# Performance work log

Hardware: AMD Instinct MI355X
Metric: run time of the kernel (lower is better)

The kernel has to match this reference:

```python
import jax, jax.numpy as jnp
import numpy as np

BATCH = 8192
N = 32
A_NUM = 5
EPS = 1e-10
ALPHA = jnp.array([0.01, 0.25, 0.5, 0.9, 0.99], dtype=jnp.float32)


def setup_inputs() -> dict:
    key = jax.random.key(0)
    ks = jax.random.split(key, 9)
    stdv = 1.0 / np.sqrt(N)
    u = lambda k, shape: jax.random.uniform(k, shape, jnp.float32, -stdv, stdv)
    L = N * (N - 1) // 2
    return {
        "inputs": jax.random.normal(ks[0], (BATCH, N, N), jnp.float32),
        "state": jax.random.normal(ks[1], (BATCH, A_NUM * N * N), jnp.float32),
        "WR_root": u(ks[2], (A_NUM,)),
        "Wt_root": u(ks[3], (1,)),
        "Wphi_root": u(ks[4], (1,)),
        "Ws_root": u(ks[5], (A_NUM,)),
        "Br": u(ks[6], (L, 1)),
        "Bt": u(ks[7], (L, 1)),
        "By": u(ks[8], (L, 1)),
    }


def _skew(Bvec, n):
    # Replicates the torch loop: row 0 is zeros; row k (k>=1) gets B[k-1 : 2k-1]
    # in its first k columns (overlapping slices of the flat parameter vector).
    b = Bvec.reshape(-1)
    r = jnp.arange(n)[:, None]
    c = jnp.arange(n)[None, :]
    idx = jnp.clip(r - 1 + c, 0, b.shape[0] - 1)  # B[k-1+j] for entry (k, j)
    L = jnp.where(c < r, b[idx], jnp.zeros((), b.dtype))
    return L - L.T


def _cayley(S, n):
    # MatrixExp in the source: (I - S)^{-1} (I + S)
    I = jnp.eye(n, dtype=S.dtype)
    return jnp.linalg.solve(I - S, I + S)


def _translate(A, Bvec, n):
    # M @ A @ M.T with M the Cayley 'exp' of the skew matrix built from Bvec.
    M = _cayley(_skew(Bvec, n), n)
    return jnp.einsum('ij,bjk,lk->bil', M, A, M)


def _nus(W_root, A, eps):
    # Weighted average over the a_num axis with weights W_root^2 / (sum + eps).
    W = W_root * W_root
    return jnp.einsum('a,banm->bnm', W / (W.sum() + eps), A)


def reference(inputs, state, WR_root, Wt_root, Wphi_root, Ws_root, Br, Bt, By):
    Mt_1 = state.reshape(-1, A_NUM, N, N)                 # [B, a, n, n]
    X = inputs.reshape(BATCH, N, N)                       # [B, n, n]

    Yt = _nus(WR_root, Mt_1, EPS)                         # [B, n, n]
    Rt = _translate(Yt, Br, N)

    at = (Wt_root[0] ** 2) / ((Wt_root ** 2 + Wphi_root ** 2).sum() + EPS)
    Tt = (1.0 - at) * X + at * Rt                         # Frechet mean FM
    Phit = _translate(Tt, Bt, N)

    # Per-j Frechet means, vectorized over the a_num axis.
    a = ALPHA[None, :, None, None]
    Mt = (1.0 - a) * Mt_1 + a * Phit[:, None, :, :]       # [B, a, n, n]

    St = _nus(Ws_root, Mt, EPS)
    Ot = _translate(St, By, N)                            # [B, n, n]

    return Ot, Mt.reshape(-1, A_NUM, N, N)
```

## Files before the change

kernel.cpp:

```cpp
#include <hip/hip_runtime.h>

#define NB 8192
#define OT_ELEMS (NB * 1024)
#define EPSF 1e-10f

typedef __attribute__((ext_vector_type(4))) float f32x4;
typedef __attribute__((ext_vector_type(8))) short s16x8;

#define WAVE_FENCE() asm volatile("s_waitcnt lgkmcnt(0)" ::: "memory")
#define MFMA_B16(A, B, C) __builtin_amdgcn_mfma_f32_16x16x32_bf16((A), (B), (C), 0, 0, 0)

__global__ void cayley_kernel(const float* __restrict__ Br,
                              const float* __restrict__ Bt,
                              const float* __restrict__ By,
                              float* __restrict__ M_out) {
  __shared__ float A[32][33];
  __shared__ float R[32][33];
  const float* B = (blockIdx.x == 0) ? Br : (blockIdx.x == 1) ? Bt : By;
  const int t = threadIdx.x;
  const int i = t >> 5, j = t & 31;
  float Lij = (j < i) ? B[i - 1 + j] : 0.0f;
  float Lji = (i < j) ? B[j - 1 + i] : 0.0f;
  float S = Lij - Lji;
  float eye = (i == j) ? 1.0f : 0.0f;
  A[i][j] = eye - S;
  R[i][j] = eye + S;
  __syncthreads();
  for (int p = 0; p < 32; ++p) {
    float f = A[i][p] / A[p][p];
    __syncthreads();
    if (i != p) {
      A[i][j] -= f * A[p][j];
      R[i][j] -= f * R[p][j];
    }
    __syncthreads();
  }
  M_out[blockIdx.x * 1024 + i * 32 + j] = R[i][j] / A[i][i];
}

__device__ __forceinline__ void cvt_hilo8(const f32x4 f0, const f32x4 f1, s16x8& hi, s16x8& lo) {
  float f[8];
#pragma unroll
  for (int e = 0; e < 4; ++e) { f[e] = f0[e]; f[4 + e] = f1[e]; }
#pragma unroll
  for (int e = 0; e < 8; ++e) {
    unsigned u = __float_as_uint(f[e]);
    hi[e] = (short)(u >> 16);
    float ah = __uint_as_float(u & 0xffff0000u);
    lo[e] = (short)(__float_as_uint(f[e] - ah) >> 16);
  }
}

__device__ __forceinline__ void read_frag_lds(const float* sb, int off, s16x8& hi, s16x8& lo) {
  f32x4 f0 = *(const f32x4*)(sb + off);
  f32x4 f1 = *(const f32x4*)(sb + off + 4);
  cvt_hilo8(f0, f1, hi, lo);
}

__device__ __forceinline__ void congruence_rt(float* sb, int lane,
                                              const s16x8 (&Mh)[2], const s16x8 (&Ml)[2],
                                              const f32x4 (&in)[4], f32x4 (&outr)[4]) {
  const int l15 = lane & 15, l4 = lane >> 4;
  const int i0 = (lane >> 3) << 2, j0 = (lane & 7) << 2;
#pragma unroll
  for (int c = 0; c < 4; ++c) {
    f32x4 colv = {in[0][c], in[1][c], in[2][c], in[3][c]};
    *(f32x4*)(sb + (j0 + c) * 36 + i0) = colv;
  }
  WAVE_FENCE();
  s16x8 Bh[2], Bl[2];
#pragma unroll
  for (int s = 0; s < 2; ++s)
    read_frag_lds(sb, (16 * s + l15) * 36 + 8 * l4, Bh[s], Bl[s]);
  WAVE_FENCE();
  f32x4 g[2][2];
#pragma unroll
  for (int ms = 0; ms < 2; ++ms)
#pragma unroll
    for (int ns = 0; ns < 2; ++ns) {
      f32x4 acc = {0.f, 0.f, 0.f, 0.f};
      acc = MFMA_B16(Ml[ms], Bh[ns], acc);
      acc = MFMA_B16(Mh[ms], Bl[ns], acc);
      acc = MFMA_B16(Mh[ms], Bh[ns], acc);
      g[ms][ns] = acc;
    }
#pragma unroll
  for (int ms = 0; ms < 2; ++ms)
#pragma unroll
    for (int ns = 0; ns < 2; ++ns)
#pragma unroll
      for (int r = 0; r < 4; ++r)
        sb[(16 * ms + 4 * l4 + r) * 36 + 16 * ns + l15] = g[ms][ns][r];
  WAVE_FENCE();
  s16x8 Ah[2], Al[2];
#pragma unroll
  for (int s = 0; s < 2; ++s)
    read_frag_lds(sb, (16 * s + l15) * 36 + 8 * l4, Ah[s], Al[s]);
  WAVE_FENCE();
  f32x4 o[2][2];
#pragma unroll
  for (int ms = 0; ms < 2; ++ms)
#pragma unroll
    for (int ns = 0; ns < 2; ++ns) {
      f32x4 acc = {0.f, 0.f, 0.f, 0.f};
      acc = MFMA_B16(Al[ms], Mh[ns], acc);
      acc = MFMA_B16(Ah[ms], Ml[ns], acc);
      acc = MFMA_B16(Ah[ms], Mh[ns], acc);
      o[ms][ns] = acc;
    }
#pragma unroll
  for (int ms = 0; ms < 2; ++ms)
#pragma unroll
    for (int ns = 0; ns < 2; ++ns)
#pragma unroll
      for (int r = 0; r < 4; ++r)
        sb[(16 * ms + 4 * l4 + r) * 36 + 16 * ns + l15] = o[ms][ns][r];
  WAVE_FENCE();
#pragma unroll
  for (int r = 0; r < 4; ++r)
    outr[r] = *(const f32x4*)(sb + (i0 + r) * 36 + j0);
  WAVE_FENCE();
}

__global__ __launch_bounds__(64) void spdsru_main(
    const float* __restrict__ X, const float* __restrict__ state,
    const float* __restrict__ WR, const float* __restrict__ Wt,
    const float* __restrict__ Wphi, const float* __restrict__ Ws,
    const float* __restrict__ Mg, float* __restrict__ out) {
  __shared__ __align__(16) float sb[1152];
  const int lane = threadIdx.x;
  const int l15 = lane & 15, l4 = lane >> 4;
  const int i0 = (lane >> 3) << 2, j0 = (lane & 7) << 2;
  const int batch = blockIdx.x;

  s16x8 Mh[3][2], Ml[3][2];
#pragma unroll
  for (int q = 0; q < 3; ++q)
#pragma unroll
    for (int s = 0; s < 2; ++s) {
      const float* p = Mg + q * 1024 + (16 * s + l15) * 32 + 8 * l4;
      cvt_hilo8(*(const f32x4*)p, *(const f32x4*)(p + 4), Mh[q][s], Ml[q][s]);
    }

  const float alpha[5] = {0.01f, 0.25f, 0.5f, 0.9f, 0.99f};
  float wr[5], va[5];
  float cP = 0.f;
  {
    float sR = 0.f, sS = 0.f, wq[5];
#pragma unroll
    for (int a = 0; a < 5; ++a) { float v = WR[a]; wr[a] = v * v; sR += v * v; }
#pragma unroll
    for (int a = 0; a < 5; ++a) { float v = Ws[a]; wq[a] = v * v; sS += v * v; }
    const float invR = 1.0f / (sR + EPSF), invS = 1.0f / (sS + EPSF);
#pragma unroll
    for (int a = 0; a < 5; ++a) {
      wr[a] *= invR;
      float w = wq[a] * invS;
      va[a] = w * (1.0f - alpha[a]);
      cP += w * alpha[a];
    }
  }
  const float wt2 = Wt[0] * Wt[0], wp2 = Wphi[0] * Wphi[0];
  const float at = wt2 / (wt2 + wp2 + EPSF);
  const float omat = 1.0f - at;

  const float* xp = X + (size_t)batch * 1024;
  f32x4 x[4];
#pragma unroll
  for (int r = 0; r < 4; ++r) x[r] = *(const f32x4*)(xp + (i0 + r) * 32 + j0);

  const float* stp = state + (size_t)batch * 5120;
  f32x4 U[4], V[4];
#pragma unroll
  for (int r = 0; r < 4; ++r) { U[r] = f32x4{0.f, 0.f, 0.f, 0.f}; V[r] = U[r]; }
#pragma unroll
  for (int a = 0; a < 5; ++a)
#pragma unroll
    for (int r = 0; r < 4; ++r) {
      const f32x4 v = *(const f32x4*)(stp + a * 1024 + (i0 + r) * 32 + j0);
      U[r] += wr[a] * v;
      V[r] += va[a] * v;
    }

  f32x4 rt[4];
  congruence_rt(sb, lane, Mh[0], Ml[0], U, rt);
  f32x4 tt[4];
#pragma unroll
  for (int r = 0; r < 4; ++r) tt[r] = omat * x[r] + at * rt[r];

  f32x4 ph[4];
  congruence_rt(sb, lane, Mh[1], Ml[1], tt, ph);

  float* outMt = out + OT_ELEMS + (size_t)batch * 5120;
#pragma unroll
  for (int a = 0; a < 5; ++a) {
    const float al = alpha[a], om = 1.0f - al;
#pragma unroll
    for (int r = 0; r < 4; ++r) {
      const f32x4 v = *(const f32x4*)(stp + a * 1024 + (i0 + r) * 32 + j0);
      f32x4 w = om * v + al * ph[r];
      *(f32x4*)(outMt + a * 1024 + (i0 + r) * 32 + j0) = w;
    }
  }

  f32x4 st[4];
#pragma unroll
  for (int r = 0; r < 4; ++r) st[r] = V[r] + cP * ph[r];
  f32x4 ot[4];
  congruence_rt(sb, lane, Mh[2], Ml[2], st, ot);

  float* outOt = out + (size_t)batch * 1024;
#pragma unroll
  for (int r = 0; r < 4; ++r)
    *(f32x4*)(outOt + (i0 + r) * 32 + j0) = ot[r];
}

extern "C" void kernel_launch(void* const* d_in, const int* in_sizes, int n_in,
                              void* d_out, int out_size, void* d_ws, size_t ws_size,
                              hipStream_t stream) {
  const float* X     = (const float*)d_in[0];
  const float* state = (const float*)d_in[1];
  const float* WR    = (const float*)d_in[2];
  const float* Wt    = (const float*)d_in[3];
  const float* Wphi  = (const float*)d_in[4];
  const float* Ws    = (const float*)d_in[5];
  const float* Br    = (const float*)d_in[6];
  const float* Bt    = (const float*)d_in[7];
  const float* By    = (const float*)d_in[8];
  float* m_ws = (float*)d_ws;
  float* outp = (float*)d_out;

  cayley_kernel<<<3, 1024, 0, stream>>>(Br, Bt, By, m_ws);
  spdsru_main<<<NB, 64, 0, stream>>>(X, state, WR, Wt, Wphi, Ws, m_ws, outp);
}
```

Baseline: 101.4 us.

## Process two batch matrices per wavefront with interleaved congruence transforms

Each 64-thread block now handles two batch entries, and the three congruence transforms run on both matrices together through two LDS buffers. This interleaves independent MFMA chains and LDS traffic, giving more instruction-level parallelism per wave and amortizing the per-block load and hi/lo split of the three M matrices. St is now accumulated from the freshly computed Mt values rather than from a precomputed V/cP decomposition. In exchange the grid is half as large, register pressure roughly doubles, and occupancy may drop.

```diff
diff --git a/kernel.cpp b/kernel.cpp
--- a/kernel.cpp
+++ b/kernel.cpp
@@ -57,68 +57,86 @@
   cvt_hilo8(f0, f1, hi, lo);
 }
 
-__device__ __forceinline__ void congruence_rt(float* sb, int lane,
-                                              const s16x8 (&Mh)[2], const s16x8 (&Ml)[2],
-                                              const f32x4 (&in)[4], f32x4 (&outr)[4]) {
+__device__ __forceinline__ void congruence2(float* __restrict__ sb0, float* __restrict__ sb1,
+                                            int lane,
+                                            const s16x8 (&Mh)[2], const s16x8 (&Ml)[2],
+                                            const f32x4 (&in0)[4], const f32x4 (&in1)[4],
+                                            f32x4 (&out0)[4], f32x4 (&out1)[4]) {
   const int l15 = lane & 15, l4 = lane >> 4;
   const int i0 = (lane >> 3) << 2, j0 = (lane & 7) << 2;
 #pragma unroll
   for (int c = 0; c < 4; ++c) {
-    f32x4 colv = {in[0][c], in[1][c], in[2][c], in[3][c]};
-    *(f32x4*)(sb + (j0 + c) * 36 + i0) = colv;
-  }
-  WAVE_FENCE();
-  s16x8 Bh[2], Bl[2];
-#pragma unroll
-  for (int s = 0; s < 2; ++s)
-    read_frag_lds(sb, (16 * s + l15) * 36 + 8 * l4, Bh[s], Bl[s]);
-  WAVE_FENCE();
-  f32x4 g[2][2];
+    f32x4 c0 = {in0[0][c], in0[1][c], in0[2][c], in0[3][c]};
+    f32x4 c1 = {in1[0][c], in1[1][c], in1[2][c], in1[3][c]};
+    *(f32x4*)(sb0 + (j0 + c) * 36 + i0) = c0;
+    *(f32x4*)(sb1 + (j0 + c) * 36 + i0) = c1;
+  }
+  WAVE_FENCE();
+  s16x8 Bh[2][2], Bl[2][2];
+#pragma unroll
+  for (int s = 0; s < 2; ++s) {
+    read_frag_lds(sb0, (16 * s + l15) * 36 + 8 * l4, Bh[0][s], Bl[0][s]);
+    read_frag_lds(sb1, (16 * s + l15) * 36 + 8 * l4, Bh[1][s], Bl[1][s]);
+  }
+  WAVE_FENCE();
+  f32x4 g[2][2][2];
+#pragma unroll
+  for (int b = 0; b < 2; ++b)
+#pragma unroll
+    for (int ms = 0; ms < 2; ++ms)
+#pragma unroll
+      for (int ns = 0; ns < 2; ++ns) {
+        f32x4 acc = {0.f, 0.f, 0.f, 0.f};
+        acc = MFMA_B16(Ml[ms], Bh[b][ns], acc);
+        acc = MFMA_B16(Mh[ms], Bl[b][ns], acc);
+        acc = MFMA_B16(Mh[ms], Bh[b][ns], acc);
+        g[b][ms][ns] = acc;
+      }
 #pragma unroll
   for (int ms = 0; ms < 2; ++ms)
 #pragma unroll
-    for (int ns = 0; ns < 2; ++ns) {
-      f32x4 acc = {0.f, 0.f, 0.f, 0.f};
-      acc = MFMA_B16(Ml[ms], Bh[ns], acc);
-      acc = MFMA_B16(Mh[ms], Bl[ns], acc);
-      acc = MFMA_B16(Mh[ms], Bh[ns], acc);
-      g[ms][ns] = acc;
-    }
+    for (int ns = 0; ns < 2; ++ns)
+#pragma unroll
+      for (int r = 0; r < 4; ++r) {
+        sb0[(16 * ms + 4 * l4 + r) * 36 + 16 * ns + l15] = g[0][ms][ns][r];
+        sb1[(16 * ms + 4 * l4 + r) * 36 + 16 * ns + l15] = g[1][ms][ns][r];
+      }
+  WAVE_FENCE();
+  s16x8 Ah[2][2], Al[2][2];
+#pragma unroll
+  for (int s = 0; s < 2; ++s) {
+    read_frag_lds(sb0, (16 * s + l15) * 36 + 8 * l4, Ah[0][s], Al[0][s]);
+    read_frag_lds(sb1, (16 * s + l15) * 36 + 8 * l4, Ah[1][s], Al[1][s]);
+  }
+  WAVE_FENCE();
+  f32x4 o[2][2][2];
+#pragma unroll
+  for (int b = 0; b < 2; ++b)
+#pragma unroll
+    for (int ms = 0; ms < 2; ++ms)
+#pragma unroll
+      for (int ns = 0; ns < 2; ++ns) {
+        f32x4 acc = {0.f, 0.f, 0.f, 0.f};
+        acc = MFMA_B16(Al[b][ms], Mh[ns], acc);
+        acc = MFMA_B16(Ah[b][ms], Ml[ns], acc);
+        acc = MFMA_B16(Ah[b][ms], Mh[ns], acc);
+        o[b][ms][ns] = acc;
+      }
 #pragma unroll
   for (int ms = 0; ms < 2; ++ms)
 #pragma unroll
     for (int ns = 0; ns < 2; ++ns)
 #pragma unroll
-      for (int r = 0; r < 4; ++r)
-        sb[(16 * ms + 4 * l4 + r) * 36 + 16 * ns + l15] = g[ms][ns][r];
-  WAVE_FENCE();
-  s16x8 Ah[2], Al[2];
-#pragma unroll
-  for (int s = 0; s < 2; ++s)
-    read_frag_lds(sb, (16 * s + l15) * 36 + 8 * l4, Ah[s], Al[s]);
-  WAVE_FENCE();
-  f32x4 o[2][2];
-#pragma unroll
-  for (int ms = 0; ms < 2; ++ms)
-#pragma unroll
-    for (int ns = 0; ns < 2; ++ns) {
-      f32x4 acc = {0.f, 0.f, 0.f, 0.f};
-      acc = MFMA_B16(Al[ms], Mh[ns], acc);
-      acc = MFMA_B16(Ah[ms], Ml[ns], acc);
-      acc = MFMA_B16(Ah[ms], Mh[ns], acc);
-      o[ms][ns] = acc;
-    }
-#pragma unroll
-  for (int ms = 0; ms < 2; ++ms)
-#pragma unroll
-    for (int ns = 0; ns < 2; ++ns)
-#pragma unroll
-      for (int r = 0; r < 4; ++r)
-        sb[(16 * ms + 4 * l4 + r) * 36 + 16 * ns + l15] = o[ms][ns][r];
-  WAVE_FENCE();
-#pragma unroll
-  for (int r = 0; r < 4; ++r)
-    outr[r] = *(const f32x4*)(sb + (i0 + r) * 36 + j0);
+      for (int r = 0; r < 4; ++r) {
+        sb0[(16 * ms + 4 * l4 + r) * 36 + 16 * ns + l15] = o[0][ms][ns][r];
+        sb1[(16 * ms + 4 * l4 + r) * 36 + 16 * ns + l15] = o[1][ms][ns][r];
+      }
+  WAVE_FENCE();
+#pragma unroll
+  for (int r = 0; r < 4; ++r) {
+    out0[r] = *(const f32x4*)(sb0 + (i0 + r) * 36 + j0);
+    out1[r] = *(const f32x4*)(sb1 + (i0 + r) * 36 + j0);
+  }
   WAVE_FENCE();
 }
 
@@ -127,11 +145,11 @@
     const float* __restrict__ WR, const float* __restrict__ Wt,
     const float* __restrict__ Wphi, const float* __restrict__ Ws,
     const float* __restrict__ Mg, float* __restrict__ out) {
-  __shared__ __align__(16) float sb[1152];
+  __shared__ __align__(16) float sb[2][1184];
   const int lane = threadIdx.x;
   const int l15 = lane & 15, l4 = lane >> 4;
   const int i0 = (lane >> 3) << 2, j0 = (lane & 7) << 2;
-  const int batch = blockIdx.x;
+  const int batch0 = blockIdx.x * 2;
 
   s16x8 Mh[3][2], Ml[3][2];
 #pragma unroll
@@ -143,76 +161,86 @@
     }
 
   const float alpha[5] = {0.01f, 0.25f, 0.5f, 0.9f, 0.99f};
-  float wr[5], va[5];
-  float cP = 0.f;
+  float wr[5], wsn[5];
   {
-    float sR = 0.f, sS = 0.f, wq[5];
+    float sR = 0.f, sS = 0.f;
 #pragma unroll
     for (int a = 0; a < 5; ++a) { float v = WR[a]; wr[a] = v * v; sR += v * v; }
 #pragma unroll
-    for (int a = 0; a < 5; ++a) { float v = Ws[a]; wq[a] = v * v; sS += v * v; }
+    for (int a = 0; a < 5; ++a) { float v = Ws[a]; wsn[a] = v * v; sS += v * v; }
     const float invR = 1.0f / (sR + EPSF), invS = 1.0f / (sS + EPSF);
 #pragma unroll
-    for (int a = 0; a < 5; ++a) {
-      wr[a] *= invR;
-      float w = wq[a] * invS;
-      va[a] = w * (1.0f - alpha[a]);
-      cP += w * alpha[a];
-    }
+    for (int a = 0; a < 5; ++a) { wr[a] *= invR; wsn[a] *= invS; }
   }
   const float wt2 = Wt[0] * Wt[0], wp2 = Wphi[0] * Wphi[0];
   const float at = wt2 / (wt2 + wp2 + EPSF);
   const float omat = 1.0f - at;
 
-  const float* xp = X + (size_t)batch * 1024;
-  f32x4 x[4];
-#pragma unroll
-  for (int r = 0; r < 4; ++r) x[r] = *(const f32x4*)(xp + (i0 + r) * 32 + j0);
-
-  const float* stp = state + (size_t)batch * 5120;
-  f32x4 U[4], V[4];
-#pragma unroll
-  for (int r = 0; r < 4; ++r) { U[r] = f32x4{0.f, 0.f, 0.f, 0.f}; V[r] = U[r]; }
+  const float* xp0 = X + (size_t)batch0 * 1024;
+  f32x4 x0[4], x1[4];
+#pragma unroll
+  for (int r = 0; r < 4; ++r) {
+    x0[r] = *(const f32x4*)(xp0 + (i0 + r) * 32 + j0);
+    x1[r] = *(const f32x4*)(xp0 + 1024 + (i0 + r) * 32 + j0);
+  }
+
+  const float* stp0 = state + (size_t)batch0 * 5120;
+  const float* stp1 = stp0 + 5120;
+  f32x4 U0[4], U1[4];
+#pragma unroll
+  for (int r = 0; r < 4; ++r) { U0[r] = f32x4{0.f, 0.f, 0.f, 0.f}; U1[r] = U0[r]; }
 #pragma unroll
   for (int a = 0; a < 5; ++a)
 #pragma unroll
     for (int r = 0; r < 4; ++r) {
-      const f32x4 v = *(const f32x4*)(stp + a * 1024 + (i0 + r) * 32 + j0);
-      U[r] += wr[a] * v;
-      V[r] += va[a] * v;
-    }
-
-  f32x4 rt[4];
-  congruence_rt(sb, lane, Mh[0], Ml[0], U, rt);
-  f32x4 tt[4];
-#pragma unroll
-  for (int r = 0; r < 4; ++r) tt[r] = omat * x[r] + at * rt[r];
-
-  f32x4 ph[4];
-  congruence_rt(sb, lane, Mh[1], Ml[1], tt, ph);
-
-  float* outMt = out + OT_ELEMS + (size_t)batch * 5120;
+      const f32x4 v0 = *(const f32x4*)(stp0 + a * 1024 + (i0 + r) * 32 + j0);
+      const f32x4 v1 = *(const f32x4*)(stp1 + a * 1024 + (i0 + r) * 32 + j0);
+      U0[r] += wr[a] * v0;
+      U1[r] += wr[a] * v1;
+    }
+
+  f32x4 rt0[4], rt1[4];
+  congruence2(sb[0], sb[1], lane, Mh[0], Ml[0], U0, U1, rt0, rt1);
+  f32x4 tt0[4], tt1[4];
+#pragma unroll
+  for (int r = 0; r < 4; ++r) {
+    tt0[r] = omat * x0[r] + at * rt0[r];
+    tt1[r] = omat * x1[r] + at * rt1[r];
+  }
+
+  f32x4 ph0[4], ph1[4];
+  congruence2(sb[0], sb[1], lane, Mh[1], Ml[1], tt0, tt1, ph0, ph1);
+
+  float* outMt0 = out + OT_ELEMS + (size_t)batch0 * 5120;
+  float* outMt1 = outMt0 + 5120;
+  f32x4 st0[4], st1[4];
+#pragma unroll
+  for (int r = 0; r < 4; ++r) { st0[r] = f32x4{0.f, 0.f, 0.f, 0.f}; st1[r] = st0[r]; }
 #pragma unroll
   for (int a = 0; a < 5; ++a) {
-    const float al = alpha[a], om = 1.0f - al;
+    const float al = alpha[a], om = 1.0f - al, ws = wsn[a];
 #pragma unroll
     for (int r = 0; r < 4; ++r) {
-      const f32x4 v = *(const f32x4*)(stp + a * 1024 + (i0 + r) * 32 + j0);
-      f32x4 w = om * v + al * ph[r];
-      *(f32x4*)(outMt + a * 1024 + (i0 + r) * 32 + j0) = w;
-    }
-  }
-
-  f32x4 st[4];
-#pragma unroll
-  for (int r = 0; r < 4; ++r) st[r] = V[r] + cP * ph[r];
-  f32x4 ot[4];
-  congruence_rt(sb, lane, Mh[2], Ml[2], st, ot);
-
-  float* outOt = out + (size_t)batch * 1024;
-#pragma unroll
-  for (int r = 0; r < 4; ++r)
-    *(f32x4*)(outOt + (i0 + r) * 32 + j0) = ot[r];
+      const f32x4 v0 = *(const f32x4*)(stp0 + a * 1024 + (i0 + r) * 32 + j0);
+      const f32x4 v1 = *(const f32x4*)(stp1 + a * 1024 + (i0 + r) * 32 + j0);
+      f32x4 w0 = om * v0 + al * ph0[r];
+      f32x4 w1 = om * v1 + al * ph1[r];
+      *(f32x4*)(outMt0 + a * 1024 + (i0 + r) * 32 + j0) = w0;
+      *(f32x4*)(outMt1 + a * 1024 + (i0 + r) * 32 + j0) = w1;
+      st0[r] += ws * w0;
+      st1[r] += ws * w1;
+    }
+  }
+
+  f32x4 ot0[4], ot1[4];
+  congruence2(sb[0], sb[1], lane, Mh[2], Ml[2], st0, st1, ot0, ot1);
+
+  float* outOt0 = out + (size_t)batch0 * 1024;
+#pragma unroll
+  for (int r = 0; r < 4; ++r) {
+    *(f32x4*)(outOt0 + (i0 + r) * 32 + j0) = ot0[r];
+    *(f32x4*)(outOt0 + 1024 + (i0 + r) * 32 + j0) = ot1[r];
+  }
 }
 
 extern "C" void kernel_launch(void* const* d_in, const int* in_sizes, int n_in,
@@ -231,5 +259,5 @@
   float* outp = (float*)d_out;
 
   cayley_kernel<<<3, 1024, 0, stream>>>(Br, Bt, By, m_ws);
-  spdsru_main<<<NB, 64, 0, stream>>>(X, state, WR, Wt, Wphi, Ws, m_ws, outp);
-}
+  spdsru_main<<<NB / 2, 64, 0, stream>>>(X, state, WR, Wt, Wphi, Ws, m_ws, outp);
+}
```

Result: slower. 104.9 us (+3.4%).

## Process four batches per block with software-prefetched state and nontemporal stores

Applied to the files above, without the earlier changes.

Each 64-thread block now handles four consecutive batch items, with a swizzled block-to-batch mapping. It prefetches the next item's state tiles into registers while the current item's congruence transforms run. It also recomputes St from the Mt values it writes instead of using precomputed V/cP, uses nontemporal loads and stores for streaming X and the outputs, and wraps the LDS waits in scheduling barriers. This aims to hide global-memory latency and amortize the per-block Cayley matrix setup, at the cost of many more registers (20 f32x4 prefetch buffers) and fewer blocks in flight.

```diff
diff --git a/kernel.cpp b/kernel.cpp
--- a/kernel.cpp
+++ b/kernel.cpp
@@ -1,13 +1,16 @@
 #include <hip/hip_runtime.h>
 
 #define NB 8192
+#define GPB 4
 #define OT_ELEMS (NB * 1024)
 #define EPSF 1e-10f
 
 typedef __attribute__((ext_vector_type(4))) float f32x4;
 typedef __attribute__((ext_vector_type(8))) short s16x8;
 
-#define WAVE_FENCE() asm volatile("s_waitcnt lgkmcnt(0)" ::: "memory")
+#define SBAR() __builtin_amdgcn_sched_barrier(0)
+#define LGK()  do { SBAR(); asm volatile("s_waitcnt lgkmcnt(0)"); SBAR(); } while (0)
+
 #define MFMA_B16(A, B, C) __builtin_amdgcn_mfma_f32_16x16x32_bf16((A), (B), (C), 0, 0, 0)
 
 __global__ void cayley_kernel(const float* __restrict__ Br,
@@ -67,12 +70,12 @@
     f32x4 colv = {in[0][c], in[1][c], in[2][c], in[3][c]};
     *(f32x4*)(sb + (j0 + c) * 36 + i0) = colv;
   }
-  WAVE_FENCE();
+  LGK();
   s16x8 Bh[2], Bl[2];
 #pragma unroll
   for (int s = 0; s < 2; ++s)
     read_frag_lds(sb, (16 * s + l15) * 36 + 8 * l4, Bh[s], Bl[s]);
-  WAVE_FENCE();
+  LGK();
   f32x4 g[2][2];
 #pragma unroll
   for (int ms = 0; ms < 2; ++ms)
@@ -91,12 +94,12 @@
 #pragma unroll
       for (int r = 0; r < 4; ++r)
         sb[(16 * ms + 4 * l4 + r) * 36 + 16 * ns + l15] = g[ms][ns][r];
-  WAVE_FENCE();
+  LGK();
   s16x8 Ah[2], Al[2];
 #pragma unroll
   for (int s = 0; s < 2; ++s)
     read_frag_lds(sb, (16 * s + l15) * 36 + 8 * l4, Ah[s], Al[s]);
-  WAVE_FENCE();
+  LGK();
   f32x4 o[2][2];
 #pragma unroll
   for (int ms = 0; ms < 2; ++ms)
@@ -115,11 +118,11 @@
 #pragma unroll
       for (int r = 0; r < 4; ++r)
         sb[(16 * ms + 4 * l4 + r) * 36 + 16 * ns + l15] = o[ms][ns][r];
-  WAVE_FENCE();
+  LGK();
 #pragma unroll
   for (int r = 0; r < 4; ++r)
     outr[r] = *(const f32x4*)(sb + (i0 + r) * 36 + j0);
-  WAVE_FENCE();
+  LGK();
 }
 
 __global__ __launch_bounds__(64) void spdsru_main(
@@ -127,11 +130,12 @@
     const float* __restrict__ WR, const float* __restrict__ Wt,
     const float* __restrict__ Wphi, const float* __restrict__ Ws,
     const float* __restrict__ Mg, float* __restrict__ out) {
-  __shared__ __align__(16) float sb[1152];
+  __shared__ __align__(16) float sb[1184];
   const int lane = threadIdx.x;
   const int l15 = lane & 15, l4 = lane >> 4;
   const int i0 = (lane >> 3) << 2, j0 = (lane & 7) << 2;
-  const int batch = blockIdx.x;
+  const int bid = blockIdx.x;
+  const int batch0 = ((bid & 7) * (NB / GPB / 8) + (bid >> 3)) * GPB;
 
   s16x8 Mh[3][2], Ml[3][2];
 #pragma unroll
@@ -143,76 +147,91 @@
     }
 
   const float alpha[5] = {0.01f, 0.25f, 0.5f, 0.9f, 0.99f};
-  float wr[5], va[5];
-  float cP = 0.f;
+  float wr[5], wsn[5];
   {
-    float sR = 0.f, sS = 0.f, wq[5];
+    float sR = 0.f, sS = 0.f;
 #pragma unroll
     for (int a = 0; a < 5; ++a) { float v = WR[a]; wr[a] = v * v; sR += v * v; }
 #pragma unroll
-    for (int a = 0; a < 5; ++a) { float v = Ws[a]; wq[a] = v * v; sS += v * v; }
+    for (int a = 0; a < 5; ++a) { float v = Ws[a]; wsn[a] = v * v; sS += v * v; }
     const float invR = 1.0f / (sR + EPSF), invS = 1.0f / (sS + EPSF);
 #pragma unroll
-    for (int a = 0; a < 5; ++a) {
-      wr[a] *= invR;
-      float w = wq[a] * invS;
-      va[a] = w * (1.0f - alpha[a]);
-      cP += w * alpha[a];
-    }
+    for (int a = 0; a < 5; ++a) { wr[a] *= invR; wsn[a] *= invS; }
   }
   const float wt2 = Wt[0] * Wt[0], wp2 = Wphi[0] * Wphi[0];
   const float at = wt2 / (wt2 + wp2 + EPSF);
   const float omat = 1.0f - at;
 
-  const float* xp = X + (size_t)batch * 1024;
-  f32x4 x[4];
-#pragma unroll
-  for (int r = 0; r < 4; ++r) x[r] = *(const f32x4*)(xp + (i0 + r) * 32 + j0);
-
-  const float* stp = state + (size_t)batch * 5120;
-  f32x4 U[4], V[4];
-#pragma unroll
-  for (int r = 0; r < 4; ++r) { U[r] = f32x4{0.f, 0.f, 0.f, 0.f}; V[r] = U[r]; }
-#pragma unroll
-  for (int a = 0; a < 5; ++a)
+  f32x4 raw[20];
+  {
+    const float* stp = state + (size_t)batch0 * 5120;
+#pragma unroll
+    for (int a = 0; a < 5; ++a)
+#pragma unroll
+      for (int r = 0; r < 4; ++r)
+        raw[a * 4 + r] = *(const f32x4*)(stp + a * 1024 + (i0 + r) * 32 + j0);
+  }
+
+#pragma unroll 1
+  for (int g = 0; g < GPB; ++g) {
+    const int batch = batch0 + g;
+    const float* stg = state + (size_t)batch * 5120;
+
+    f32x4 U[4];
 #pragma unroll
     for (int r = 0; r < 4; ++r) {
-      const f32x4 v = *(const f32x4*)(stp + a * 1024 + (i0 + r) * 32 + j0);
-      U[r] += wr[a] * v;
-      V[r] += va[a] * v;
-    }
-
-  f32x4 rt[4];
-  congruence_rt(sb, lane, Mh[0], Ml[0], U, rt);
-  f32x4 tt[4];
-#pragma unroll
-  for (int r = 0; r < 4; ++r) tt[r] = omat * x[r] + at * rt[r];
-
-  f32x4 ph[4];
-  congruence_rt(sb, lane, Mh[1], Ml[1], tt, ph);
-
-  float* outMt = out + OT_ELEMS + (size_t)batch * 5120;
-#pragma unroll
-  for (int a = 0; a < 5; ++a) {
-    const float al = alpha[a], om = 1.0f - al;
-#pragma unroll
-    for (int r = 0; r < 4; ++r) {
-      const f32x4 v = *(const f32x4*)(stp + a * 1024 + (i0 + r) * 32 + j0);
-      f32x4 w = om * v + al * ph[r];
-      *(f32x4*)(outMt + a * 1024 + (i0 + r) * 32 + j0) = w;
-    }
-  }
-
-  f32x4 st[4];
-#pragma unroll
-  for (int r = 0; r < 4; ++r) st[r] = V[r] + cP * ph[r];
-  f32x4 ot[4];
-  congruence_rt(sb, lane, Mh[2], Ml[2], st, ot);
-
-  float* outOt = out + (size_t)batch * 1024;
-#pragma unroll
-  for (int r = 0; r < 4; ++r)
-    *(f32x4*)(outOt + (i0 + r) * 32 + j0) = ot[r];
+      f32x4 u = wr[0] * raw[r];
+#pragma unroll
+      for (int a = 1; a < 5; ++a) u += wr[a] * raw[a * 4 + r];
+      U[r] = u;
+    }
+
+    const float* xp = X + (size_t)batch * 1024;
+    f32x4 x[4];
+#pragma unroll
+    for (int r = 0; r < 4; ++r)
+      x[r] = __builtin_nontemporal_load((const f32x4*)(xp + (i0 + r) * 32 + j0));
+    if (g + 1 < GPB) {
+      const float* stn = stg + 5120;
+#pragma unroll
+      for (int a = 0; a < 5; ++a)
+#pragma unroll
+        for (int r = 0; r < 4; ++r)
+          raw[a * 4 + r] = *(const f32x4*)(stn + a * 1024 + (i0 + r) * 32 + j0);
+    }
+
+    f32x4 rt[4];
+    congruence_rt(sb, lane, Mh[0], Ml[0], U, rt);
+    f32x4 tt[4];
+#pragma unroll
+    for (int r = 0; r < 4; ++r) tt[r] = omat * x[r] + at * rt[r];
+
+    f32x4 ph[4];
+    congruence_rt(sb, lane, Mh[1], Ml[1], tt, ph);
+
+    float* outMt = out + OT_ELEMS + (size_t)batch * 5120;
+    f32x4 st[4];
+#pragma unroll
+    for (int r = 0; r < 4; ++r) st[r] = f32x4{0.f, 0.f, 0.f, 0.f};
+#pragma unroll
+    for (int a = 0; a < 5; ++a) {
+      const float al = alpha[a], om = 1.0f - al, ws = wsn[a];
+#pragma unroll
+      for (int r = 0; r < 4; ++r) {
+        const f32x4 v = *(const f32x4*)(stg + a * 1024 + (i0 + r) * 32 + j0);
+        f32x4 w = om * v + al * ph[r];
+        __builtin_nontemporal_store(w, (f32x4*)(outMt + a * 1024 + (i0 + r) * 32 + j0));
+        st[r] += ws * w;
+      }
+    }
+
+    f32x4 ot[4];
+    congruence_rt(sb, lane, Mh[2], Ml[2], st, ot);
+    float* outOt = out + (size_t)batch * 1024;
+#pragma unroll
+    for (int r = 0; r < 4; ++r)
+      __builtin_nontemporal_store(ot[r], (f32x4*)(outOt + (i0 + r) * 32 + j0));
+  }
 }
 
 extern "C" void kernel_launch(void* const* d_in, const int* in_sizes, int n_in,
@@ -231,5 +250,5 @@
   float* outp = (float*)d_out;
 
   cayley_kernel<<<3, 1024, 0, stream>>>(Br, Bt, By, m_ws);
-  spdsru_main<<<NB, 64, 0, stream>>>(X, state, WR, Wt, Wphi, Ws, m_ws, outp);
-}
+  spdsru_main<<<NB / GPB, 64, 0, stream>>>(X, state, WR, Wt, Wphi, Ws, m_ws, outp);
+}
```

After: 114.1 us. 1.13x slower.

## Fold two congruences into one via precomputed Mt·Mr and interleave independent paths

Applied to the files above, without the earlier changes.

Since Phi = Mt(omat·X + at·Mr U Mr^T)Mt^T, the change precomputes Mt·Mr in a new tiny kernel and computes Mt X Mt^T and (MtMr) U (MtMr)^T in parallel, removing the serial dependency between the first two congruences. It also remaps block indices to batches, reloads state into registers ahead of the last congruence, uses nontemporal loads and stores, and wraps the LDS waits in sched barriers. The work is about the same (four transforms instead of three congruence passes), so it trades some extra MFMA work and register pressure for more instruction-level parallelism. It also adds one more kernel launch and slightly changes rounding.

```diff
diff --git a/kernel.cpp b/kernel.cpp
--- a/kernel.cpp
+++ b/kernel.cpp
@@ -7,7 +7,9 @@
 typedef __attribute__((ext_vector_type(4))) float f32x4;
 typedef __attribute__((ext_vector_type(8))) short s16x8;
 
-#define WAVE_FENCE() asm volatile("s_waitcnt lgkmcnt(0)" ::: "memory")
+#define SBAR() __builtin_amdgcn_sched_barrier(0)
+#define LGK()  do { SBAR(); asm volatile("s_waitcnt lgkmcnt(0)"); SBAR(); } while (0)
+
 #define MFMA_B16(A, B, C) __builtin_amdgcn_mfma_f32_16x16x32_bf16((A), (B), (C), 0, 0, 0)
 
 __global__ void cayley_kernel(const float* __restrict__ Br,
@@ -38,6 +40,20 @@
   M_out[blockIdx.x * 1024 + i * 32 + j] = R[i][j] / A[i][i];
 }
 
+__global__ void combine_kernel(float* __restrict__ ws) {
+  __shared__ float sMR[1024], sMT[1024];
+  const int t = threadIdx.x;
+  sMR[t] = ws[t];
+  sMT[t] = ws[1024 + t];
+  __syncthreads();
+  const int i = t >> 5, j = t & 31;
+  float s = 0.f;
+#pragma unroll
+  for (int k = 0; k < 32; ++k)
+    s = fmaf(sMT[i * 32 + k], sMR[k * 32 + j], s);
+  ws[3072 + i * 32 + j] = s;
+}
+
 __device__ __forceinline__ void cvt_hilo8(const f32x4 f0, const f32x4 f1, s16x8& hi, s16x8& lo) {
   float f[8];
 #pragma unroll
@@ -57,90 +73,30 @@
   cvt_hilo8(f0, f1, hi, lo);
 }
 
-__device__ __forceinline__ void congruence_rt(float* sb, int lane,
-                                              const s16x8 (&Mh)[2], const s16x8 (&Ml)[2],
-                                              const f32x4 (&in)[4], f32x4 (&outr)[4]) {
-  const int l15 = lane & 15, l4 = lane >> 4;
-  const int i0 = (lane >> 3) << 2, j0 = (lane & 7) << 2;
-#pragma unroll
-  for (int c = 0; c < 4; ++c) {
-    f32x4 colv = {in[0][c], in[1][c], in[2][c], in[3][c]};
-    *(f32x4*)(sb + (j0 + c) * 36 + i0) = colv;
-  }
-  WAVE_FENCE();
-  s16x8 Bh[2], Bl[2];
-#pragma unroll
-  for (int s = 0; s < 2; ++s)
-    read_frag_lds(sb, (16 * s + l15) * 36 + 8 * l4, Bh[s], Bl[s]);
-  WAVE_FENCE();
-  f32x4 g[2][2];
-#pragma unroll
-  for (int ms = 0; ms < 2; ++ms)
-#pragma unroll
-    for (int ns = 0; ns < 2; ++ns) {
-      f32x4 acc = {0.f, 0.f, 0.f, 0.f};
-      acc = MFMA_B16(Ml[ms], Bh[ns], acc);
-      acc = MFMA_B16(Mh[ms], Bl[ns], acc);
-      acc = MFMA_B16(Mh[ms], Bh[ns], acc);
-      g[ms][ns] = acc;
-    }
-#pragma unroll
-  for (int ms = 0; ms < 2; ++ms)
-#pragma unroll
-    for (int ns = 0; ns < 2; ++ns)
-#pragma unroll
-      for (int r = 0; r < 4; ++r)
-        sb[(16 * ms + 4 * l4 + r) * 36 + 16 * ns + l15] = g[ms][ns][r];
-  WAVE_FENCE();
-  s16x8 Ah[2], Al[2];
-#pragma unroll
-  for (int s = 0; s < 2; ++s)
-    read_frag_lds(sb, (16 * s + l15) * 36 + 8 * l4, Ah[s], Al[s]);
-  WAVE_FENCE();
-  f32x4 o[2][2];
-#pragma unroll
-  for (int ms = 0; ms < 2; ++ms)
-#pragma unroll
-    for (int ns = 0; ns < 2; ++ns) {
-      f32x4 acc = {0.f, 0.f, 0.f, 0.f};
-      acc = MFMA_B16(Al[ms], Mh[ns], acc);
-      acc = MFMA_B16(Ah[ms], Ml[ns], acc);
-      acc = MFMA_B16(Ah[ms], Mh[ns], acc);
-      o[ms][ns] = acc;
-    }
-#pragma unroll
-  for (int ms = 0; ms < 2; ++ms)
-#pragma unroll
-    for (int ns = 0; ns < 2; ++ns)
-#pragma unroll
-      for (int r = 0; r < 4; ++r)
-        sb[(16 * ms + 4 * l4 + r) * 36 + 16 * ns + l15] = o[ms][ns][r];
-  WAVE_FENCE();
-#pragma unroll
-  for (int r = 0; r < 4; ++r)
-    outr[r] = *(const f32x4*)(sb + (i0 + r) * 36 + j0);
-  WAVE_FENCE();
-}
-
 __global__ __launch_bounds__(64) void spdsru_main(
     const float* __restrict__ X, const float* __restrict__ state,
     const float* __restrict__ WR, const float* __restrict__ Wt,
     const float* __restrict__ Wphi, const float* __restrict__ Ws,
     const float* __restrict__ Mg, float* __restrict__ out) {
-  __shared__ __align__(16) float sb[1152];
+  __shared__ __align__(16) float sb0[1184];
+  __shared__ __align__(16) float sb1[1184];
   const int lane = threadIdx.x;
   const int l15 = lane & 15, l4 = lane >> 4;
   const int i0 = (lane >> 3) << 2, j0 = (lane & 7) << 2;
-  const int batch = blockIdx.x;
+  const int bid = blockIdx.x;
+  const int batch = (bid & 7) * (NB >> 3) + (bid >> 3);
 
   s16x8 Mh[3][2], Ml[3][2];
-#pragma unroll
-  for (int q = 0; q < 3; ++q)
-#pragma unroll
-    for (int s = 0; s < 2; ++s) {
-      const float* p = Mg + q * 1024 + (16 * s + l15) * 32 + 8 * l4;
-      cvt_hilo8(*(const f32x4*)p, *(const f32x4*)(p + 4), Mh[q][s], Ml[q][s]);
-    }
+  {
+    const int srcoff[3] = {1024, 3072, 2048};
+#pragma unroll
+    for (int q = 0; q < 3; ++q)
+#pragma unroll
+      for (int s = 0; s < 2; ++s) {
+        const float* p = Mg + srcoff[q] + (16 * s + l15) * 32 + 8 * l4;
+        cvt_hilo8(*(const f32x4*)p, *(const f32x4*)(p + 4), Mh[q][s], Ml[q][s]);
+      }
+  }
 
   const float alpha[5] = {0.01f, 0.25f, 0.5f, 0.9f, 0.99f};
   float wr[5], va[5];
@@ -167,7 +123,8 @@
   const float* xp = X + (size_t)batch * 1024;
   f32x4 x[4];
 #pragma unroll
-  for (int r = 0; r < 4; ++r) x[r] = *(const f32x4*)(xp + (i0 + r) * 32 + j0);
+  for (int r = 0; r < 4; ++r)
+    x[r] = __builtin_nontemporal_load((const f32x4*)(xp + (i0 + r) * 32 + j0));
 
   const float* stp = state + (size_t)batch * 5120;
   f32x4 U[4], V[4];
@@ -182,37 +139,164 @@
       V[r] += va[a] * v;
     }
 
-  f32x4 rt[4];
-  congruence_rt(sb, lane, Mh[0], Ml[0], U, rt);
-  f32x4 tt[4];
-#pragma unroll
-  for (int r = 0; r < 4; ++r) tt[r] = omat * x[r] + at * rt[r];
-
-  f32x4 ph[4];
-  congruence_rt(sb, lane, Mh[1], Ml[1], tt, ph);
-
+#pragma unroll
+  for (int c = 0; c < 4; ++c) {
+    f32x4 cx = {x[0][c], x[1][c], x[2][c], x[3][c]};
+    f32x4 cu = {U[0][c], U[1][c], U[2][c], U[3][c]};
+    *(f32x4*)(sb0 + (j0 + c) * 36 + i0) = cx;
+    *(f32x4*)(sb1 + (j0 + c) * 36 + i0) = cu;
+  }
+  LGK();
+  s16x8 BXh[2], BXl[2], BUh[2], BUl[2];
+#pragma unroll
+  for (int s = 0; s < 2; ++s) {
+    read_frag_lds(sb0, (16 * s + l15) * 36 + 8 * l4, BXh[s], BXl[s]);
+    read_frag_lds(sb1, (16 * s + l15) * 36 + 8 * l4, BUh[s], BUl[s]);
+  }
+  LGK();
+  f32x4 gX[2][2], gU[2][2];
+#pragma unroll
+  for (int ms = 0; ms < 2; ++ms)
+#pragma unroll
+    for (int ns = 0; ns < 2; ++ns) {
+      f32x4 a0 = {0.f, 0.f, 0.f, 0.f};
+      a0 = MFMA_B16(Ml[0][ms], BXh[ns], a0);
+      a0 = MFMA_B16(Mh[0][ms], BXl[ns], a0);
+      a0 = MFMA_B16(Mh[0][ms], BXh[ns], a0);
+      gX[ms][ns] = a0;
+      f32x4 a1 = {0.f, 0.f, 0.f, 0.f};
+      a1 = MFMA_B16(Ml[1][ms], BUh[ns], a1);
+      a1 = MFMA_B16(Mh[1][ms], BUl[ns], a1);
+      a1 = MFMA_B16(Mh[1][ms], BUh[ns], a1);
+      gU[ms][ns] = a1;
+    }
+#pragma unroll
+  for (int ms = 0; ms < 2; ++ms)
+#pragma unroll
+    for (int ns = 0; ns < 2; ++ns)
+#pragma unroll
+      for (int r = 0; r < 4; ++r) {
+        sb0[(16 * ms + 4 * l4 + r) * 36 + 16 * ns + l15] = gX[ms][ns][r];
+        sb1[(16 * ms + 4 * l4 + r) * 36 + 16 * ns + l15] = gU[ms][ns][r];
+      }
+  LGK();
+  s16x8 AXh[2], AXl[2], AUh[2], AUl[2];
+#pragma unroll
+  for (int s = 0; s < 2; ++s) {
+    read_frag_lds(sb0, (16 * s + l15) * 36 + 8 * l4, AXh[s], AXl[s]);
+    read_frag_lds(sb1, (16 * s + l15) * 36 + 8 * l4, AUh[s], AUl[s]);
+  }
+  LGK();
+  f32x4 ph[2][2];
+#pragma unroll
+  for (int ms = 0; ms < 2; ++ms)
+#pragma unroll
+    for (int ns = 0; ns < 2; ++ns) {
+      f32x4 a0 = {0.f, 0.f, 0.f, 0.f};
+      a0 = MFMA_B16(AXl[ms], Mh[0][ns], a0);
+      a0 = MFMA_B16(AXh[ms], Ml[0][ns], a0);
+      a0 = MFMA_B16(AXh[ms], Mh[0][ns], a0);
+      f32x4 a1 = {0.f, 0.f, 0.f, 0.f};
+      a1 = MFMA_B16(AUl[ms], Mh[1][ns], a1);
+      a1 = MFMA_B16(AUh[ms], Ml[1][ns], a1);
+      a1 = MFMA_B16(AUh[ms], Mh[1][ns], a1);
+      ph[ms][ns] = omat * a0 + at * a1;
+    }
+
+#pragma unroll
+  for (int ms = 0; ms < 2; ++ms)
+#pragma unroll
+    for (int ns = 0; ns < 2; ++ns)
+#pragma unroll
+      for (int r = 0; r < 4; ++r)
+        sb0[(16 * ms + 4 * l4 + r) * 36 + 16 * ns + l15] = ph[ms][ns][r];
+  LGK();
+  f32x4 ph4[4];
+#pragma unroll
+  for (int r = 0; r < 4; ++r)
+    ph4[r] = *(const f32x4*)(sb0 + (i0 + r) * 36 + j0);
+  LGK();
+
+  f32x4 st4[4];
+#pragma unroll
+  for (int r = 0; r < 4; ++r) st4[r] = V[r] + cP * ph4[r];
+#pragma unroll
+  for (int c = 0; c < 4; ++c) {
+    f32x4 cs = {st4[0][c], st4[1][c], st4[2][c], st4[3][c]};
+    *(f32x4*)(sb0 + (j0 + c) * 36 + i0) = cs;
+  }
+  f32x4 raw[20];
+#pragma unroll
+  for (int a = 0; a < 5; ++a)
+#pragma unroll
+    for (int r = 0; r < 4; ++r)
+      raw[a * 4 + r] = *(const f32x4*)(stp + a * 1024 + (i0 + r) * 32 + j0);
+  LGK();
+
+  s16x8 BSh[2], BSl[2];
+#pragma unroll
+  for (int s = 0; s < 2; ++s)
+    read_frag_lds(sb0, (16 * s + l15) * 36 + 8 * l4, BSh[s], BSl[s]);
+  LGK();
+  f32x4 gS[2][2];
+#pragma unroll
+  for (int ms = 0; ms < 2; ++ms)
+#pragma unroll
+    for (int ns = 0; ns < 2; ++ns) {
+      f32x4 acc = {0.f, 0.f, 0.f, 0.f};
+      acc = MFMA_B16(Ml[2][ms], BSh[ns], acc);
+      acc = MFMA_B16(Mh[2][ms], BSl[ns], acc);
+      acc = MFMA_B16(Mh[2][ms], BSh[ns], acc);
+      gS[ms][ns] = acc;
+    }
   float* outMt = out + OT_ELEMS + (size_t)batch * 5120;
 #pragma unroll
   for (int a = 0; a < 5; ++a) {
     const float al = alpha[a], om = 1.0f - al;
 #pragma unroll
     for (int r = 0; r < 4; ++r) {
-      const f32x4 v = *(const f32x4*)(stp + a * 1024 + (i0 + r) * 32 + j0);
-      f32x4 w = om * v + al * ph[r];
-      *(f32x4*)(outMt + a * 1024 + (i0 + r) * 32 + j0) = w;
-    }
-  }
-
-  f32x4 st[4];
-#pragma unroll
-  for (int r = 0; r < 4; ++r) st[r] = V[r] + cP * ph[r];
-  f32x4 ot[4];
-  congruence_rt(sb, lane, Mh[2], Ml[2], st, ot);
-
+      f32x4 w = om * raw[a * 4 + r] + al * ph4[r];
+      __builtin_nontemporal_store(w, (f32x4*)(outMt + a * 1024 + (i0 + r) * 32 + j0));
+    }
+  }
+#pragma unroll
+  for (int ms = 0; ms < 2; ++ms)
+#pragma unroll
+    for (int ns = 0; ns < 2; ++ns)
+#pragma unroll
+      for (int r = 0; r < 4; ++r)
+        sb0[(16 * ms + 4 * l4 + r) * 36 + 16 * ns + l15] = gS[ms][ns][r];
+  LGK();
+  s16x8 ASh[2], ASl[2];
+#pragma unroll
+  for (int s = 0; s < 2; ++s)
+    read_frag_lds(sb0, (16 * s + l15) * 36 + 8 * l4, ASh[s], ASl[s]);
+  LGK();
+  f32x4 o[2][2];
+#pragma unroll
+  for (int ms = 0; ms < 2; ++ms)
+#pragma unroll
+    for (int ns = 0; ns < 2; ++ns) {
+      f32x4 acc = {0.f, 0.f, 0.f, 0.f};
+      acc = MFMA_B16(ASl[ms], Mh[2][ns], acc);
+      acc = MFMA_B16(ASh[ms], Ml[2][ns], acc);
+      acc = MFMA_B16(ASh[ms], Mh[2][ns], acc);
+      o[ms][ns] = acc;
+    }
+#pragma unroll
+  for (int ms = 0; ms < 2; ++ms)
+#pragma unroll
+    for (int ns = 0; ns < 2; ++ns)
+#pragma unroll
+      for (int r = 0; r < 4; ++r)
+        sb0[(16 * ms + 4 * l4 + r) * 36 + 16 * ns + l15] = o[ms][ns][r];
+  LGK();
   float* outOt = out + (size_t)batch * 1024;
 #pragma unroll
-  for (int r = 0; r < 4; ++r)
-    *(f32x4*)(outOt + (i0 + r) * 32 + j0) = ot[r];
+  for (int r = 0; r < 4; ++r) {
+    f32x4 ov = *(const f32x4*)(sb0 + (i0 + r) * 36 + j0);
+    __builtin_nontemporal_store(ov, (f32x4*)(outOt + (i0 + r) * 32 + j0));
+  }
 }
 
 extern "C" void kernel_launch(void* const* d_in, const int* in_sizes, int n_in,
@@ -231,5 +315,6 @@
   float* outp = (float*)d_out;
 
   cayley_kernel<<<3, 1024, 0, stream>>>(Br, Bt, By, m_ws);
+  combine_kernel<<<1, 1024, 0, stream>>>(m_ws);
   spdsru_main<<<NB, 64, 0, stream>>>(X, state, WR, Wt, Wphi, Ws, m_ws, outp);
 }
```

New measurement: 89.09 us. -12.1%, faster.
